# Kernel tuning notes

Measured on AMD Instinct MI355X. Metric: run time of the kernel, lower is better.

## Reference

```python
import jax, jax.numpy as jnp
import numpy as np

B, N, HW, PS, FHW = 16, 4096, 224, 8, 56

def _gelu(x):
    return jax.nn.gelu(x, approximate=True)  # tanh approximation, matches nn.GELU(approximate='tanh')

def _conv(x, w, b, stride):
    y = jax.lax.conv_general_dilated(x, w, (stride, stride), [(1, 1), (1, 1)],
                                     dimension_numbers=('NCHW', 'OIHW', 'NCHW'))
    return y + b[None, :, None, None]

def _embed(points):
    # for i in 0..11: append sin(2^i * p) then cos(2^i * p) -> [B,N,48]
    factors = 2.0 ** jnp.arange(12, dtype=points.dtype)
    scaled = points[..., None, :] * factors[:, None]          # [B,N,12,2]
    feats = jnp.concatenate([jnp.sin(scaled), jnp.cos(scaled)], axis=-1)  # [B,N,12,4]
    return feats.reshape(points.shape[0], points.shape[1], 48)

def _extract_patches(fmap, points):
    # fmap [B,C,H,W]; points in [0,1]; bilinear grid_sample, zeros padding, align_corners=True
    Bq, C, H, W = fmap.shape
    centers = points * 2.0 - 1.0
    step = 2.0 / (W - 1)
    half = (PS - 1) / 2.0
    offs = jnp.linspace(-half, half, PS, dtype=fmap.dtype) * step
    offx2d, offy2d = jnp.meshgrid(offs, offs, indexing='ij')   # [ps,ps]
    gx = centers[..., 0][..., None, None] + offx2d             # [B,N,ps,ps]
    gy = centers[..., 1][..., None, None] + offy2d
    # align_corners=True pixel coords
    ix = (gx + 1.0) * 0.5 * (W - 1)
    iy = (gy + 1.0) * 0.5 * (H - 1)
    x0f = jnp.floor(ix); y0f = jnp.floor(iy)
    x0 = x0f.astype(jnp.int32); y0 = y0f.astype(jnp.int32)
    x1 = x0 + 1; y1 = y0 + 1
    wx1 = ix - x0f; wx0 = 1.0 - wx1
    wy1 = iy - y0f; wy0 = 1.0 - wy1
    fflat = fmap.reshape(Bq, C, H * W)

    def corner(xi, yi, w):
        valid = ((xi >= 0) & (xi < W) & (yi >= 0) & (yi < H)).astype(fmap.dtype)
        idx = jnp.clip(yi, 0, H - 1) * W + jnp.clip(xi, 0, W - 1)   # [B,N,ps,ps]
        vals = jax.vmap(lambda f, i: f[:, i])(fflat, idx)           # [B,C,N,ps,ps]
        return vals * (w * valid)[:, None]

    out = (corner(x0, y0, wx0 * wy0) + corner(x1, y0, wx1 * wy0)
           + corner(x0, y1, wx0 * wy1) + corner(x1, y1, wx1 * wy1))  # [B,C,N,ps,ps]
    return out.transpose(0, 2, 1, 3, 4)                              # [B,N,C,ps,ps]

def setup_inputs():
    key = jax.random.key(0)
    ks = jax.random.split(key, 26)
    def w(k, shape):
        fan_in = int(np.prod(shape[1:]))
        return jax.random.normal(k, shape, jnp.float32) * (1.0 / np.sqrt(fan_in))
    inp = {
        'points': jax.random.uniform(ks[0], (B, N, 2), jnp.float32),
        'images': jax.random.normal(ks[1], (B, 3, HW, HW), jnp.float32),
        # plane encoder
        'pw1': w(ks[2], (16, 3, 3, 3)),  'pb1': jnp.zeros((16,), jnp.float32),
        'pw2': w(ks[3], (32, 16, 3, 3)), 'pb2': jnp.zeros((32,), jnp.float32),
        'pw3': w(ks[4], (4, 32, 3, 3)),  'pb3': jnp.zeros((4,), jnp.float32),
        # global encoder
        'gw1': w(ks[5], (4, 3, 3, 3)),   'gb1': jnp.zeros((4,), jnp.float32),
        'gw2': w(ks[6], (8, 4, 3, 3)),   'gb2': jnp.zeros((8,), jnp.float32),
        'gw3': w(ks[7], (16, 8, 3, 3)),  'gb3': jnp.zeros((16,), jnp.float32),
        'gw4': w(ks[8], (32, 16, 3, 3)), 'gb4': jnp.zeros((32,), jnp.float32),
        'gw5': w(ks[9], (64, 32, 3, 3)), 'gb5': jnp.zeros((64,), jnp.float32),
        # point encoder (torch Linear: [out,in])
        'lw1': w(ks[10], (256, 48)),  'lb1': jnp.zeros((256,), jnp.float32),
        'lw2': w(ks[11], (256, 256)), 'lb2': jnp.zeros((256,), jnp.float32),
        # head
        'hw1': w(ks[12], (512, 576)), 'hb1': jnp.zeros((512,), jnp.float32),
        'hw2': w(ks[13], (1, 512)),   'hb2': jnp.zeros((1,), jnp.float32),
    }
    return inp

def reference(points, images, pw1, pb1, pw2, pb2, pw3, pb3,
              gw1, gb1, gw2, gb2, gw3, gb3, gw4, gb4, gw5, gb5,
              lw1, lb1, lw2, lb2, hw1, hb1, hw2, hb2):
    # point branch
    pe = _embed(points)                                         # [B,N,48]
    pf = _gelu(pe @ lw1.T + lb1) @ lw2.T + lb2                  # [B,N,256]
    # plane encoder -> 4x56x56 fmap
    f = _gelu(_conv(images, pw1, pb1, 2))
    f = _gelu(_conv(f, pw2, pb2, 2))
    fmap = _gelu(_conv(f, pw3, pb3, 1))                         # [B,4,56,56]
    # global encoder -> [B,64]
    g = images
    for wg, bg in ((gw1, gb1), (gw2, gb2), (gw3, gb3), (gw4, gb4), (gw5, gb5)):
        g = _gelu(_conv(g, wg, bg, 2))
    gc = g.mean(axis=(2, 3))                                    # AvgPool2d(7)+Flatten -> [B,64]
    gc = jnp.broadcast_to(gc[:, None, :], (points.shape[0], points.shape[1], 64))
    # per-point bilinear patch gather
    patches = _extract_patches(fmap, points).reshape(points.shape[0], points.shape[1], -1)  # [B,N,256]
    fused = jnp.concatenate([pf, patches, gc], axis=-1)         # [B,N,576]
    logit = _gelu(fused @ hw1.T + hb1) @ hw2.T + hb2            # [B,N,1]
    return logit
```

## Files before the change

kernel.cpp:

```cpp
#include <hip/hip_runtime.h>
#include <math.h>

#define BB 16
#define NN 4096
#define M_TOT (BB*NN)

typedef __attribute__((ext_vector_type(8))) short s8v;
typedef __attribute__((ext_vector_type(4))) float f4v;

__device__ __forceinline__ float gelu_t(float x){
    float u = 1.5957691216057308f * x * (1.0f + 0.044715f*x*x);
    return x / (1.0f + __expf(-u));
}

__device__ __forceinline__ unsigned short f2bf(float f){
    unsigned int u = __float_as_uint(f);
    u += 0x7fffu + ((u >> 16) & 1u);
    return (unsigned short)(u >> 16);
}

#define GLL(src, dst) __builtin_amdgcn_global_load_lds( \
    (const __attribute__((address_space(1))) void*)(src), \
    (__attribute__((address_space(3))) void*)(dst), 16, 0, 0)

template<int CIN, int COUT, int STRIDE, int CHUNK>
__device__ __forceinline__ void conv_dev2(
    const float* __restrict__ in, const float* __restrict__ w,
    const float* __restrict__ bias, float* __restrict__ out,
    int Hin, int Win, int Hout, int Wout, int bx, int by, int b, float* tile)
{
    constexpr int IW = 15*STRIDE + 3;
    constexpr int IH = IW;
    constexpr int PITCH = IW + 1;
    int tid = threadIdx.x;
    int tx = tid & 15, ty = tid >> 4;
    int wo = bx*16 + tx;
    int ho = by*16 + ty;
    int win0 = bx*16*STRIDE - 1;
    int hin0 = by*16*STRIDE - 1;
    bool valid = (wo < Wout) && (ho < Hout);

    float acc[COUT];
    #pragma unroll
    for (int co = 0; co < COUT; ++co) acc[co] = bias[co];

    const float* ib = in + (size_t)(b*CIN)*Hin*Win;
    for (int ci0 = 0; ci0 < CIN; ci0 += CHUNK) {
        __syncthreads();
        for (int idx = tid; idx < CHUNK*IH*IW; idx += 256) {
            int c = idx / (IH*IW), rem = idx - c*(IH*IW);
            int r = rem / IW, cc = rem - r*IW;
            int hi = hin0 + r, wi = win0 + cc;
            float v = 0.f;
            if ((unsigned)hi < (unsigned)Hin && (unsigned)wi < (unsigned)Win)
                v = ib[(size_t)(ci0 + c)*Hin*Win + hi*Win + wi];
            tile[c*IH*PITCH + r*PITCH + cc] = v;
        }
        __syncthreads();
        for (int ci = 0; ci < CHUNK; ++ci) {
            float vv[9];
            const float* tb = tile + ci*IH*PITCH;
            #pragma unroll
            for (int kh = 0; kh < 3; ++kh)
                #pragma unroll
                for (int kw = 0; kw < 3; ++kw)
                    vv[kh*3+kw] = tb[(ty*STRIDE + kh)*PITCH + tx*STRIDE + kw];
            const float* wc = w + (ci0 + ci)*9;
            #pragma unroll
            for (int co = 0; co < COUT; ++co) {
                const float* wp = wc + co*CIN*9;
                #pragma unroll
                for (int k = 0; k < 9; ++k)
                    acc[co] = fmaf(vv[k], wp[k], acc[co]);
            }
        }
    }
    if (valid) {
        size_t obase = ((size_t)b*COUT)*Hout*Wout + (size_t)ho*Wout + wo;
        #pragma unroll
        for (int co = 0; co < COUT; ++co)
            out[obase + (size_t)co*Hout*Wout] = gelu_t(acc[co]);
    }
}

__global__ __launch_bounds__(256) void conv_dual_k(
    const float* __restrict__ in,
    const float* __restrict__ wA, const float* __restrict__ bA,
    const float* __restrict__ wB, const float* __restrict__ bB,
    float* __restrict__ outA, float* __restrict__ outB)
{
    __shared__ float tile[3*33*34];
    const int Hin = 224, Win = 224, Hout = 112, Wout = 112;
    int tid = threadIdx.x;
    int tx = tid & 15, ty = tid >> 4;
    int b = blockIdx.z;
    int wo = blockIdx.x*16 + tx;
    int ho = blockIdx.y*16 + ty;
    int win0 = blockIdx.x*32 - 1;
    int hin0 = blockIdx.y*32 - 1;

    const float* ib = in + (size_t)(b*3)*Hin*Win;
    for (int idx = tid; idx < 3*1089; idx += 256) {
        int c = idx / 1089, rem = idx - c*1089;
        int r = rem / 33, cc = rem - r*33;
        int hi = hin0 + r, wi = win0 + cc;
        float v = 0.f;
        if ((unsigned)hi < (unsigned)Hin && (unsigned)wi < (unsigned)Win)
            v = ib[(size_t)c*Hin*Win + hi*Win + wi];
        tile[c*33*34 + r*34 + cc] = v;
    }
    __syncthreads();

    float accA[16], accB[4];
    #pragma unroll
    for (int co = 0; co < 16; ++co) accA[co] = bA[co];
    #pragma unroll
    for (int co = 0; co < 4; ++co) accB[co] = bB[co];

    #pragma unroll
    for (int ci = 0; ci < 3; ++ci) {
        float vv[9];
        const float* tb = tile + ci*33*34;
        #pragma unroll
        for (int kh = 0; kh < 3; ++kh)
            #pragma unroll
            for (int kw = 0; kw < 3; ++kw)
                vv[kh*3+kw] = tb[(ty*2 + kh)*34 + tx*2 + kw];
        #pragma unroll
        for (int co = 0; co < 16; ++co) {
            const float* wp = wA + co*27 + ci*9;
            #pragma unroll
            for (int k = 0; k < 9; ++k) accA[co] = fmaf(vv[k], wp[k], accA[co]);
        }
        #pragma unroll
        for (int co = 0; co < 4; ++co) {
            const float* wp = wB + co*27 + ci*9;
            #pragma unroll
            for (int k = 0; k < 9; ++k) accB[co] = fmaf(vv[k], wp[k], accB[co]);
        }
    }
    size_t px = (size_t)ho*Wout + wo;
    #pragma unroll
    for (int co = 0; co < 16; ++co)
        outA[((size_t)(b*16 + co))*Hout*Wout + px] = gelu_t(accA[co]);
    #pragma unroll
    for (int co = 0; co < 4; ++co)
        outB[((size_t)(b*4 + co))*Hout*Wout + px] = gelu_t(accB[co]);
}

__global__ __launch_bounds__(256) void conv_pg2_k(
    const float* __restrict__ f1, const float* __restrict__ pw2, const float* __restrict__ pb2, float* __restrict__ f2,
    const float* __restrict__ g1, const float* __restrict__ gw2, const float* __restrict__ gb2, float* __restrict__ g2)
{
    __shared__ float tile[8*33*34];
    int z = blockIdx.z;
    if (z < 32) {
        int b = z >> 1, half = z & 1;
        conv_dev2<16,16,2,8>(f1 + (size_t)b*16*12544, pw2 + half*2304, pb2 + half*16,
                             f2 + ((size_t)(b*32 + half*16))*3136,
                             112,112, 56,56, blockIdx.x, blockIdx.y, 0, tile);
    } else {
        conv_dev2<4,8,2,4>(g1, gw2, gb2, g2, 112,112, 56,56, blockIdx.x, blockIdx.y, z-32, tile);
    }
}

__global__ __launch_bounds__(256) void conv_pg3_k(
    const float* __restrict__ f2, const float* __restrict__ pw3, const float* __restrict__ pb3, float4* __restrict__ fmap4,
    const float* __restrict__ g2, const float* __restrict__ gw3, const float* __restrict__ gb3, float* __restrict__ g3)
{
    __shared__ float tile[8*33*34];
    int z = blockIdx.z;
    if (z < 16) {
        int b = z;
        int idx = blockIdx.x*256 + threadIdx.x;
        if (idx >= 3136) return;
        int ho = idx / 56, wo = idx - ho*56;
        const float* ib = f2 + (size_t)b*32*3136;
        float acc[4];
        #pragma unroll
        for (int co = 0; co < 4; ++co) acc[co] = pb3[co];
        for (int ci = 0; ci < 32; ++ci) {
            const float* ic = ib + (size_t)ci*3136;
            #pragma unroll
            for (int kh = 0; kh < 3; ++kh) {
                int hi = ho - 1 + kh;
                if ((unsigned)hi >= 56u) continue;
                #pragma unroll
                for (int kw = 0; kw < 3; ++kw) {
                    int wi = wo - 1 + kw;
                    if ((unsigned)wi >= 56u) continue;
                    float v = ic[hi*56 + wi];
                    int wofs = ci*9 + kh*3 + kw;
                    #pragma unroll
                    for (int co = 0; co < 4; ++co)
                        acc[co] = fmaf(v, pw3[co*288 + wofs], acc[co]);
                }
            }
        }
        float4 o;
        o.x = gelu_t(acc[0]); o.y = gelu_t(acc[1]);
        o.z = gelu_t(acc[2]); o.w = gelu_t(acc[3]);
        fmap4[(size_t)b*3136 + idx] = o;
    } else {
        if (blockIdx.x >= 4) return;
        int bx = blockIdx.x & 1, by = blockIdx.x >> 1;
        conv_dev2<8,16,2,8>(g2, gw3, gb3, g3, 56,56, 28,28, bx, by, z-16, tile);
    }
}

__global__ __launch_bounds__(256) void k4_k(
    const float* __restrict__ g3, const float* __restrict__ w4,
    const float* __restrict__ b4, float* __restrict__ g4o,
    const float4* __restrict__ fmap4, const float* __restrict__ points,
    unsigned short* __restrict__ C)
{
    __shared__ float4 pt[4*81];
    int bid = blockIdx.x;
    int tid = threadIdx.x;
    if (bid < 392) {
        int idx = bid*256 + tid;
        int co = idx & 31;
        int t = idx >> 5;
        int b = t / 196, px = t - b*196;
        int ho = px / 14, wo = px - ho*14;
        const float* src = g3 + (size_t)b*16*784;
        const float* wp = w4 + co*144;
        float acc = b4[co];
        for (int ci = 0; ci < 16; ++ci) {
            #pragma unroll
            for (int kh = 0; kh < 3; ++kh) {
                int hi = ho*2 - 1 + kh;
                if ((unsigned)hi >= 28u) continue;
                #pragma unroll
                for (int kw = 0; kw < 3; ++kw) {
                    int wi = wo*2 - 1 + kw;
                    if ((unsigned)wi >= 28u) continue;
                    acc = fmaf(src[ci*784 + hi*28 + wi], wp[ci*9 + kh*3 + kw], acc);
                }
            }
        }
        g4o[(size_t)b*6272 + px*32 + co] = gelu_t(acc);
    } else {
        int task = (bid - 392)*256 + tid;
        int wv = tid >> 6, lane = tid & 63;
        size_t m = (size_t)(task >> 6);
        int ij = task & 63;
        int i = ij >> 3, j = ij & 7;
        int b = (int)(m >> 12);
        float px = points[m*2], py = points[m*2+1];
        float X = fmaf(px, 55.f, -3.5f);
        float Y = fmaf(py, 55.f, -3.5f);
        float xbf = floorf(X), ybf = floorf(Y);
        int xbase = (int)xbf, ybase = (int)ybf;
        float wx1 = X - xbf, wx0 = 1.f - wx1;
        float wy1 = Y - ybf, wy0 = 1.f - wy1;
        const float4* fb = fmap4 + (size_t)b*3136;
        float4* tp = pt + wv*81;

        {
            int r = lane / 9, c = lane - r*9;
            int y = ybase + r, x = xbase + c;
            float4 v = {0.f, 0.f, 0.f, 0.f};
            if ((unsigned)x < 56u && (unsigned)y < 56u) v = fb[y*56 + x];
            tp[lane] = v;
            int idx2 = 64 + lane;
            if (idx2 < 81) {
                int r2 = idx2 / 9, c2 = idx2 - r2*9;
                int y2 = ybase + r2, x2 = xbase + c2;
                float4 v2 = {0.f, 0.f, 0.f, 0.f};
                if ((unsigned)x2 < 56u && (unsigned)y2 < 56u) v2 = fb[y2*56 + x2];
                tp[idx2] = v2;
            }
        }
        __syncthreads();

        float4 f00 = tp[j*9 + i];
        float4 f10 = tp[j*9 + i + 1];
        float4 f01 = tp[j*9 + 9 + i];
        float4 f11 = tp[j*9 + 9 + i + 1];
        float4 v;
        v.x = wy0*(wx0*f00.x + wx1*f10.x) + wy1*(wx0*f01.x + wx1*f11.x);
        v.y = wy0*(wx0*f00.y + wx1*f10.y) + wy1*(wx0*f01.y + wx1*f11.y);
        v.z = wy0*(wx0*f00.z + wx1*f10.z) + wy1*(wx0*f01.z + wx1*f11.z);
        v.w = wy0*(wx0*f00.w + wx1*f10.w) + wy1*(wx0*f01.w + wx1*f11.w);
        ushort4 o;
        o.x = f2bf(v.x); o.y = f2bf(v.y); o.z = f2bf(v.z); o.w = f2bf(v.w);
        *(ushort4*)(C + m*512 + 256 + ij*4) = o;
    }
}

__global__ __launch_bounds__(256) void g5_k(
    const float* __restrict__ g4o, const float* __restrict__ w5,
    const float* __restrict__ b5, float* __restrict__ gc)
{
    int idx = blockIdx.x*256 + threadIdx.x;
    int co = idx & 63;
    int t = idx >> 6;
    int b = t / 49, px = t - b*49;
    int ho = px / 7, wo = px - ho*7;
    const float* src = g4o + (size_t)b*6272;
    const float* wp = w5 + co*288;
    float acc = b5[co];
    for (int ci = 0; ci < 32; ++ci) {
        #pragma unroll
        for (int kh = 0; kh < 3; ++kh) {
            int hi = ho*2 - 1 + kh;
            if ((unsigned)hi >= 14u) continue;
            #pragma unroll
            for (int kw = 0; kw < 3; ++kw) {
                int wi = wo*2 - 1 + kw;
                if ((unsigned)wi >= 14u) continue;
                acc = fmaf(src[(hi*14 + wi)*32 + ci], wp[ci*9 + kh*3 + kw], acc);
            }
        }
    }
    atomicAdd(&gc[b*64 + co], gelu_t(acc) * (1.0f/49.0f));
}

__global__ __launch_bounds__(256) void hgc_k(
    const float* __restrict__ gc, const float* __restrict__ hw1,
    const float* __restrict__ hb1, float* __restrict__ hgc)
{
    int idx = blockIdx.x*256 + threadIdx.x;
    int b = idx >> 9, n = idx & 511;
    const float* g = gc + b*64;
    const float* w = hw1 + (size_t)n*576 + 512;
    float s = hb1[n];
    #pragma unroll
    for (int c = 0; c < 64; ++c) s = fmaf(g[c], w[c], s);
    hgc[idx] = s;
}

__global__ void cvtall_k(const float* __restrict__ lw1, const float* __restrict__ lw2,
                         const float* __restrict__ hw1, unsigned short* __restrict__ blw1,
                         unsigned short* __restrict__ blw2, unsigned short* __restrict__ bhw1,
                         float* __restrict__ out, const float* __restrict__ b2,
                         float* __restrict__ gc){
    int i = blockIdx.x*blockDim.x + threadIdx.x;
    if (i < M_TOT) out[i] = b2[0];
    if (i < 1024) gc[i] = 0.f;
    if (i < 256*64) {
        int r = i >> 6, c = i & 63;
        blw1[i] = (c < 48) ? f2bf(lw1[r*48 + c]) : 0;
        return;
    }
    int j = i - 256*64;
    if (j < 256*256) { blw2[j] = f2bf(lw2[j]); return; }
    j -= 256*256;
    if (j < 512*576) {
        int n = j / 576, k = j - n*576;
        int src_k = k;
        if (k >= 256 && k < 512) {
            int s = k - 256;
            src_k = 256 + (s & 3)*64 + (s >> 2);
        }
        bhw1[j] = f2bf(hw1[(size_t)n*576 + src_k]);
    }
}

__global__ __launch_bounds__(512) void mlp12_k(
    const float* __restrict__ points,
    const unsigned short* __restrict__ W1, const float* __restrict__ b1,
    const unsigned short* __restrict__ W2, const float* __restrict__ b2,
    unsigned short* __restrict__ C)
{
    __shared__ unsigned short Pe[128*64];
    __shared__ unsigned short Hd[128*256];
    int tid = threadIdx.x;
    int wv = tid >> 6, lane = tid & 63;
    int q = lane >> 4, lr = lane & 15;
    int mi = wv >> 2, ni = wv & 3;
    size_t m0 = (size_t)blockIdx.x * 128;

    #pragma unroll
    for (int it = 0; it < 2; ++it) {
        int idx = it*512 + tid;
        int row = idx >> 3, seg = idx & 7;
        size_t m = m0 + row;
        float px = points[m*2], py = points[m*2+1];
        union { s8v v; unsigned short u[8]; } pk;
        #pragma unroll
        for (int j = 0; j < 8; ++j) {
            int k = seg*8 + j;
            unsigned short val = 0;
            if (k < 48) {
                int i2 = k >> 2, rr = k & 3;
                float f = (float)(1 << i2);
                float p = (rr & 1) ? py : px;
                float s = f * p;
                val = f2bf((rr < 2) ? __sinf(s) : __cosf(s));
            }
            pk.u[j] = val;
        }
        *(s8v*)(Pe + (row*8 + (seg ^ (row & 7)))*8) = pk.v;
    }
    __syncthreads();

    f4v acc1[4][4];
    #pragma unroll
    for (int i = 0; i < 4; ++i)
        #pragma unroll
        for (int j = 0; j < 4; ++j) acc1[i][j] = (f4v){0.f,0.f,0.f,0.f};

    #pragma unroll
    for (int kb = 0; kb < 2; ++kb) {
        int seg = kb*4 + q;
        s8v a[4], b[4];
        #pragma unroll
        for (int t = 0; t < 4; ++t) {
            int row = mi*64 + t*16 + lr;
            a[t] = *(const s8v*)(Pe + (row*8 + (seg ^ (row & 7)))*8);
        }
        #pragma unroll
        for (int t = 0; t < 4; ++t) {
            int n = ni*64 + t*16 + lr;
            b[t] = *(const s8v*)(W1 + n*64 + seg*8);
        }
        #pragma unroll
        for (int mt = 0; mt < 4; ++mt)
            #pragma unroll
            for (int nt = 0; nt < 4; ++nt)
                acc1[mt][nt] = __builtin_amdgcn_mfma_f32_16x16x32_bf16(a[mt], b[nt], acc1[mt][nt], 0, 0, 0);
    }
    {
        float b1v[4];
        #pragma unroll
        for (int nt = 0; nt < 4; ++nt) b1v[nt] = b1[ni*64 + nt*16 + lr];
        #pragma unroll
        for (int mt = 0; mt < 4; ++mt)
            #pragma unroll
            for (int r4 = 0; r4 < 4; ++r4) {
                int row = mi*64 + mt*16 + q*4 + r4;
                #pragma unroll
                for (int nt = 0; nt < 4; ++nt) {
                    int col = ni*64 + nt*16 + lr;
                    float v = gelu_t(acc1[mt][nt][r4] + b1v[nt]);
                    int p = (col >> 3) ^ (row & 7);
                    Hd[(row*32 + p)*8 + (col & 7)] = f2bf(v);
                }
            }
    }
    __syncthreads();

    f4v acc2[4][4];
    #pragma unroll
    for (int i = 0; i < 4; ++i)
        #pragma unroll
        for (int j = 0; j < 4; ++j) acc2[i][j] = (f4v){0.f,0.f,0.f,0.f};

    #pragma unroll 2
    for (int kt = 0; kt < 8; ++kt) {
        s8v a[4], b[4];
        #pragma unroll
        for (int t = 0; t < 4; ++t) {
            int n = ni*64 + t*16 + lr;
            b[t] = *(const s8v*)(W2 + (size_t)n*256 + kt*32 + q*8);
        }
        #pragma unroll
        for (int t = 0; t < 4; ++t) {
            int row = mi*64 + t*16 + lr;
            int p = (kt*4 + q) ^ (row & 7);
            a[t] = *(const s8v*)(Hd + (row*32 + p)*8);
        }
        #pragma unroll
        for (int mt = 0; mt < 4; ++mt)
            #pragma unroll
            for (int nt = 0; nt < 4; ++nt)
                acc2[mt][nt] = __builtin_amdgcn_mfma_f32_16x16x32_bf16(a[mt], b[nt], acc2[mt][nt], 0, 0, 0);
    }
    {
        float b2v[4];
        #pragma unroll
        for (int nt = 0; nt < 4; ++nt) b2v[nt] = b2[ni*64 + nt*16 + lr];
        #pragma unroll
        for (int mt = 0; mt < 4; ++mt)
            #pragma unroll
            for (int r4 = 0; r4 < 4; ++r4) {
                size_t m = m0 + mi*64 + mt*16 + q*4 + r4;
                #pragma unroll
                for (int nt = 0; nt < 4; ++nt) {
                    int n = ni*64 + nt*16 + lr;
                    C[m*512 + n] = f2bf(acc2[mt][nt][r4] + b2v[nt]);
                }
            }
    }
}

__global__ __launch_bounds__(512, 2) void gemm_hd_k(
    const unsigned short* __restrict__ A,
    const unsigned short* __restrict__ W,
    const float* __restrict__ hgc, const float* __restrict__ w2,
    float* __restrict__ out)
{
    __shared__ unsigned short As[2][256*64];
    __shared__ unsigned short Bs[2][256*64];
    __shared__ float red[4][256];
    int tid = threadIdx.x;
    int wv = tid >> 6, lane = tid & 63;
    int q = lane >> 4, lr = lane & 15;
    int wm = wv >> 2, wn = wv & 3;
    size_t m0 = (size_t)blockIdx.x * 256;
    int nbase = blockIdx.y * 256;
    int bimg = (int)(m0 >> 12);

    float bv[4], w2v[4];
    #pragma unroll
    for (int nt = 0; nt < 4; ++nt) {
        int n = nbase + wn*64 + nt*16 + lr;
        bv[nt] = hgc[bimg*512 + n];
        w2v[nt] = w2[n];
    }
    asm volatile("s_waitcnt vmcnt(0)" ::: "memory");

    const unsigned short* srcA[4]; int dA[4];
    const unsigned short* srcB[4]; int dB[4];
    #pragma unroll
    for (int r = 0; r < 4; ++r) {
        int f = r*512 + tid;
        int row = f >> 3, sl = (f & 7) ^ (row & 7);
        srcA[r] = A + (m0 + row)*512 + sl*8;
        srcB[r] = W + (size_t)(nbase + row)*576 + sl*8;
        dA[r] = f*8; dB[r] = f*8;
    }

    int aoff[8], boff[4];
    #pragma unroll
    for (int t = 0; t < 8; ++t) {
        int rowA = wm*128 + t*16 + lr;
        aoff[t] = (rowA*8 + (q ^ (rowA & 7)))*8;
    }
    #pragma unroll
    for (int t = 0; t < 4; ++t) {
        int rowB = wn*64 + t*16 + lr;
        boff[t] = (rowB*8 + (q ^ (rowB & 7)))*8;
    }

    f4v acc[8][4];
    #pragma unroll
    for (int i = 0; i < 8; ++i)
        #pragma unroll
        for (int j = 0; j < 4; ++j) acc[i][j] = (f4v){0.f,0.f,0.f,0.f};

    auto STAGE = [&](int buf, int ks) {
        #pragma unroll
        for (int r = 0; r < 4; ++r) GLL(srcA[r] + ks*64, &As[buf][dA[r]]);
        #pragma unroll
        for (int r = 0; r < 4; ++r) GLL(srcB[r] + ks*64, &Bs[buf][dB[r]]);
    };
    auto COMPUTE = [&](int buf) {
        #pragma unroll
        for (int kk = 0; kk < 2; ++kk) {
            s8v a[8], b[4];
            #pragma unroll
            for (int t = 0; t < 8; ++t) a[t] = *(const s8v*)(&As[buf][aoff[t] ^ (kk*32)]);
            #pragma unroll
            for (int t = 0; t < 4; ++t) b[t] = *(const s8v*)(&Bs[buf][boff[t] ^ (kk*32)]);
            #pragma unroll
            for (int mt = 0; mt < 8; ++mt)
                #pragma unroll
                for (int nt = 0; nt < 4; ++nt)
                    acc[mt][nt] = __builtin_amdgcn_mfma_f32_16x16x32_bf16(a[mt], b[nt], acc[mt][nt], 0, 0, 0);
        }
    };

    STAGE(0, 0);
    #pragma unroll
    for (int t = 0; t < 8; ++t) {
        const int cur = t & 1;
        if (t < 7) {
            STAGE(cur ^ 1, t + 1);
            asm volatile("s_waitcnt vmcnt(8)" ::: "memory");
        } else {
            asm volatile("s_waitcnt vmcnt(0)" ::: "memory");
        }
        __builtin_amdgcn_s_barrier();
        __builtin_amdgcn_sched_barrier(0);
        __builtin_amdgcn_s_setprio(1);
        COMPUTE(cur);
        __builtin_amdgcn_s_setprio(0);
        __builtin_amdgcn_sched_barrier(0);
        __builtin_amdgcn_s_barrier();
    }

    #pragma unroll
    for (int mt = 0; mt < 8; ++mt)
        #pragma unroll
        for (int r4 = 0; r4 < 4; ++r4) {
            int ml = mt*16 + q*4 + r4;
            float s = 0.f;
            #pragma unroll
            for (int nt = 0; nt < 4; ++nt)
                s += gelu_t(acc[mt][nt][r4] + bv[nt]) * w2v[nt];
            #pragma unroll
            for (int off = 8; off > 0; off >>= 1) s += __shfl_down(s, off, 16);
            if (lr == 0) red[wn][wm*128 + ml] = s;
        }
    __syncthreads();
    if (tid < 256) {
        float t = red[0][tid] + red[1][tid] + red[2][tid] + red[3][tid];
        atomicAdd(&out[m0 + tid], t);
    }
}

extern "C" void kernel_launch(void* const* d_in, const int* in_sizes, int n_in,
                              void* d_out, int out_size, void* d_ws, size_t ws_size,
                              hipStream_t stream) {
    const float* points = (const float*)d_in[0];
    const float* images = (const float*)d_in[1];
    const float* pw1 = (const float*)d_in[2];  const float* pb1 = (const float*)d_in[3];
    const float* pw2 = (const float*)d_in[4];  const float* pb2 = (const float*)d_in[5];
    const float* pw3 = (const float*)d_in[6];  const float* pb3 = (const float*)d_in[7];
    const float* gw1 = (const float*)d_in[8];  const float* gb1 = (const float*)d_in[9];
    const float* gw2 = (const float*)d_in[10]; const float* gb2 = (const float*)d_in[11];
    const float* gw3 = (const float*)d_in[12]; const float* gb3 = (const float*)d_in[13];
    const float* gw4 = (const float*)d_in[14]; const float* gb4 = (const float*)d_in[15];
    const float* gw5 = (const float*)d_in[16]; const float* gb5 = (const float*)d_in[17];
    const float* lw1 = (const float*)d_in[18]; const float* lb1 = (const float*)d_in[19];
    const float* lw2 = (const float*)d_in[20]; const float* lb2 = (const float*)d_in[21];
    const float* hw1 = (const float*)d_in[22]; const float* hb1 = (const float*)d_in[23];
    const float* hw2 = (const float*)d_in[24]; const float* hb2 = (const float*)d_in[25];
    float* out = (float*)d_out;

    char* base = (char*)d_ws;
    unsigned short* fused_b = (unsigned short*)base;
    float4* fmap4 = (float4*)(fused_b + (size_t)M_TOT*512);
    float* g3   = (float*)(fmap4 + (size_t)16*3136);
    float* g4o  = g3 + (size_t)16*16*784;
    float* gc   = g4o + (size_t)16*32*196;
    float* hgc  = gc + 1024;
    unsigned short* blw1 = (unsigned short*)(hgc + 16*512);
    unsigned short* blw2 = blw1 + 256*64;
    unsigned short* bhw1 = blw2 + 256*256;
    float* ct = (float*)base;
    float* f1 = ct;
    float* f2 = f1 + (size_t)16*16*112*112;
    float* g1 = f2 + (size_t)16*32*56*56;
    float* g2 = g1 + (size_t)16*4*112*112;

    cvtall_k<<<1472, 256, 0, stream>>>(lw1, lw2, hw1, blw1, blw2, bhw1, out, hb2, gc);
    conv_dual_k<<<dim3(7,7,16), 256, 0, stream>>>(images, pw1, pb1, gw1, gb1, f1, g1);
    conv_pg2_k<<<dim3(4,4,48), 256, 0, stream>>>(f1, pw2, pb2, f2, g1, gw2, gb2, g2);
    conv_pg3_k<<<dim3(13,1,32), 256, 0, stream>>>(f2, pw3, pb3, fmap4, g2, gw3, gb3, g3);
    k4_k<<<392 + 16384, 256, 0, stream>>>(g3, gw4, gb4, g4o, fmap4, points, fused_b);
    g5_k<<<196, 256, 0, stream>>>(g4o, gw5, gb5, gc);
    hgc_k<<<32, 256, 0, stream>>>(gc, hw1, hb1, hgc);
    mlp12_k<<<M_TOT/128, 512, 0, stream>>>(points, blw1, lb1, blw2, lb2, fused_b);
    gemm_hd_k<<<dim3(M_TOT/256, 2), 512, 0, stream>>>(fused_b, bhw1, hgc, hw2, out);
}
```

Baseline: 393.7 us.

## Single-buffer head GEMM, replace patch block barrier with wave-local wait, split g5

Head GEMM drops LDS double buffering in favour of a single buffer with load-sync-compute-sync per k-step, halving LDS so more blocks fit per CU, at the cost of exposing global load latency. The patch gather swaps a block-wide barrier for an lgkmcnt wait, since each wave only reads its own LDS tile. g5 uses 128-thread blocks over twice as many blocks. Bias and w2 loads move after the main loop.

```diff
diff --git a/kernel.cpp b/kernel.cpp
--- a/kernel.cpp
+++ b/kernel.cpp
@@ -272,7 +272,8 @@
                 tp[idx2] = v2;
             }
         }
-        __syncthreads();
+        asm volatile("s_waitcnt lgkmcnt(0)" ::: "memory");
+        __builtin_amdgcn_sched_barrier(0);
 
         float4 f00 = tp[j*9 + i];
         float4 f10 = tp[j*9 + i + 1];
@@ -289,11 +290,11 @@
     }
 }
 
-__global__ __launch_bounds__(256) void g5_k(
+__global__ __launch_bounds__(128) void g5_k(
     const float* __restrict__ g4o, const float* __restrict__ w5,
     const float* __restrict__ b5, float* __restrict__ gc)
 {
-    int idx = blockIdx.x*256 + threadIdx.x;
+    int idx = blockIdx.x*128 + threadIdx.x;
     int co = idx & 63;
     int t = idx >> 6;
     int b = t / 49, px = t - b*49;
@@ -492,8 +493,8 @@
     const float* __restrict__ hgc, const float* __restrict__ w2,
     float* __restrict__ out)
 {
-    __shared__ unsigned short As[2][256*64];
-    __shared__ unsigned short Bs[2][256*64];
+    __shared__ unsigned short As[256*64];
+    __shared__ unsigned short Bs[256*64];
     __shared__ float red[4][256];
     int tid = threadIdx.x;
     int wv = tid >> 6, lane = tid & 63;
@@ -503,15 +504,6 @@
     int nbase = blockIdx.y * 256;
     int bimg = (int)(m0 >> 12);
 
-    float bv[4], w2v[4];
-    #pragma unroll
-    for (int nt = 0; nt < 4; ++nt) {
-        int n = nbase + wn*64 + nt*16 + lr;
-        bv[nt] = hgc[bimg*512 + n];
-        w2v[nt] = w2[n];
-    }
-    asm volatile("s_waitcnt vmcnt(0)" ::: "memory");
-
     const unsigned short* srcA[4]; int dA[4];
     const unsigned short* srcB[4]; int dB[4];
     #pragma unroll
@@ -541,47 +533,41 @@
         #pragma unroll
         for (int j = 0; j < 4; ++j) acc[i][j] = (f4v){0.f,0.f,0.f,0.f};
 
-    auto STAGE = [&](int buf, int ks) {
-        #pragma unroll
-        for (int r = 0; r < 4; ++r) GLL(srcA[r] + ks*64, &As[buf][dA[r]]);
-        #pragma unroll
-        for (int r = 0; r < 4; ++r) GLL(srcB[r] + ks*64, &Bs[buf][dB[r]]);
-    };
-    auto COMPUTE = [&](int buf) {
-        #pragma unroll
-        for (int kk = 0; kk < 2; ++kk) {
-            s8v a[8], b[4];
-            #pragma unroll
-            for (int t = 0; t < 8; ++t) a[t] = *(const s8v*)(&As[buf][aoff[t] ^ (kk*32)]);
-            #pragma unroll
-            for (int t = 0; t < 4; ++t) b[t] = *(const s8v*)(&Bs[buf][boff[t] ^ (kk*32)]);
-            #pragma unroll
-            for (int mt = 0; mt < 8; ++mt)
-                #pragma unroll
-                for (int nt = 0; nt < 4; ++nt)
-                    acc[mt][nt] = __builtin_amdgcn_mfma_f32_16x16x32_bf16(a[mt], b[nt], acc[mt][nt], 0, 0, 0);
-        }
-    };
-
-    STAGE(0, 0);
-    #pragma unroll
-    for (int t = 0; t < 8; ++t) {
-        const int cur = t & 1;
-        if (t < 7) {
-            STAGE(cur ^ 1, t + 1);
-            asm volatile("s_waitcnt vmcnt(8)" ::: "memory");
-        } else {
-            asm volatile("s_waitcnt vmcnt(0)" ::: "memory");
-        }
-        __builtin_amdgcn_s_barrier();
-        __builtin_amdgcn_sched_barrier(0);
-        __builtin_amdgcn_s_setprio(1);
-        COMPUTE(cur);
-        __builtin_amdgcn_s_setprio(0);
-        __builtin_amdgcn_sched_barrier(0);
-        __builtin_amdgcn_s_barrier();
-    }
-
+#define HD_KSTEP(KS) { \
+    GLL(srcA[0] + (KS)*64, As + dA[0]); GLL(srcA[1] + (KS)*64, As + dA[1]); \
+    GLL(srcA[2] + (KS)*64, As + dA[2]); GLL(srcA[3] + (KS)*64, As + dA[3]); \
+    GLL(srcB[0] + (KS)*64, Bs + dB[0]); GLL(srcB[1] + (KS)*64, Bs + dB[1]); \
+    GLL(srcB[2] + (KS)*64, Bs + dB[2]); GLL(srcB[3] + (KS)*64, Bs + dB[3]); \
+    __syncthreads(); \
+    __builtin_amdgcn_s_setprio(1); \
+    _Pragma("unroll") \
+    for (int kk = 0; kk < 2; ++kk) { \
+        s8v a[8], b[4]; \
+        _Pragma("unroll") \
+        for (int t = 0; t < 8; ++t) a[t] = *(const s8v*)(As + (aoff[t] ^ (kk*32))); \
+        _Pragma("unroll") \
+        for (int t = 0; t < 4; ++t) b[t] = *(const s8v*)(Bs + (boff[t] ^ (kk*32))); \
+        _Pragma("unroll") \
+        for (int mt = 0; mt < 8; ++mt) \
+            _Pragma("unroll") \
+            for (int nt = 0; nt < 4; ++nt) \
+                acc[mt][nt] = __builtin_amdgcn_mfma_f32_16x16x32_bf16(a[mt], b[nt], acc[mt][nt], 0, 0, 0); \
+    } \
+    __builtin_amdgcn_s_setprio(0); \
+    __syncthreads(); \
+}
+
+    HD_KSTEP(0) HD_KSTEP(1) HD_KSTEP(2) HD_KSTEP(3)
+    HD_KSTEP(4) HD_KSTEP(5) HD_KSTEP(6) HD_KSTEP(7)
+#undef HD_KSTEP
+
+    float bv[4], w2v[4];
+    #pragma unroll
+    for (int nt = 0; nt < 4; ++nt) {
+        int n = nbase + wn*64 + nt*16 + lr;
+        bv[nt] = hgc[bimg*512 + n];
+        w2v[nt] = w2[n];
+    }
     #pragma unroll
     for (int mt = 0; mt < 8; ++mt)
         #pragma unroll
@@ -642,7 +628,7 @@
     conv_pg2_k<<<dim3(4,4,48), 256, 0, stream>>>(f1, pw2, pb2, f2, g1, gw2, gb2, g2);
     conv_pg3_k<<<dim3(13,1,32), 256, 0, stream>>>(f2, pw3, pb3, fmap4, g2, gw3, gb3, g3);
     k4_k<<<392 + 16384, 256, 0, stream>>>(g3, gw4, gb4, g4o, fmap4, points, fused_b);
-    g5_k<<<196, 256, 0, stream>>>(g4o, gw5, gb5, gc);
+    g5_k<<<392, 128, 0, stream>>>(g4o, gw5, gb5, gc);
     hgc_k<<<32, 256, 0, stream>>>(gc, hw1, hb1, hgc);
     mlp12_k<<<M_TOT/128, 512, 0, stream>>>(points, blw1, lb1, blw2, lb2, fused_b);
     gemm_hd_k<<<dim3(M_TOT/256, 2), 512, 0, stream>>>(fused_b, bhw1, hgc, hw2, out);
```

New measurement: 405.1 us. +2.9%, slower.
